# Performance work log

Hardware: AMD Instinct MI355X
Metric: run time of the kernel (lower is better)

The kernel has to match this reference:

```python
import jax, jax.numpy as jnp
import numpy as np

LAYER_NUM = 2
NUM_CLS = 128
HIDDEN = 256
NUM_NODES = 1024


def setup_inputs() -> dict:
    key = jax.random.key(0)
    ks = jax.random.split(key, 12)
    s = 0.05
    return {
        "x": jax.random.normal(ks[0], (NUM_NODES, HIDDEN), jnp.float32),
        "knowledge": jax.random.uniform(ks[1], (NUM_CLS, NUM_CLS), jnp.float32) / NUM_CLS,
        "w3w": jax.random.normal(ks[2], (HIDDEN, 2 * HIDDEN), jnp.float32) * s,
        "b3w": jax.random.normal(ks[3], (HIDDEN,), jnp.float32) * s,
        "u3": jax.random.normal(ks[4], (HIDDEN, HIDDEN), jnp.float32) * s,
        "bu3": jax.random.normal(ks[5], (HIDDEN,), jnp.float32) * s,
        "w4w": jax.random.normal(ks[6], (HIDDEN, 2 * HIDDEN), jnp.float32) * s,
        "b4w": jax.random.normal(ks[7], (HIDDEN,), jnp.float32) * s,
        "w5w": jax.random.normal(ks[8], (HIDDEN, 2 * HIDDEN), jnp.float32) * s,
        "b5w": jax.random.normal(ks[9], (HIDDEN,), jnp.float32) * s,
        "u5": jax.random.normal(ks[10], (HIDDEN, HIDDEN), jnp.float32) * s,
        "bu5": jax.random.normal(ks[11], (HIDDEN,), jnp.float32) * s,
    }


def reference(x, knowledge, w3w, b3w, u3, bu3, w4w, b4w, w5w, b5w, u5, bu5):
    N, H = x.shape
    C = knowledge.shape[0]
    # hidden[n, c, :] = x[n, :]  (repeat per class)
    hidden = jnp.broadcast_to(x[:, None, :], (N, C, H))
    for _ in range(LAYER_NUM):
        hs = hidden.sum(0)                      # [C, H]
        diff = hs[None, :, :] - hidden          # [N, C, H]
        # knowledge.T @ diff_n  and  knowledge @ diff_n, vectorized over nodes
        left = jnp.einsum('kc,nkh->nch', knowledge, diff)
        right = jnp.einsum('ck,nkh->nch', knowledge, diff)
        av = jnp.concatenate([left, right], axis=-1).reshape(N * C, 2 * H)
        h = hidden.reshape(N * C, H)
        uh3 = h @ u3.T + bu3                    # shared: rv uses fc_eq3_u (source quirk)
        zv = jax.nn.sigmoid(av @ w3w.T + b3w + uh3)
        rv = jax.nn.sigmoid(av @ w4w.T + b4w + uh3)
        hv = jnp.tanh(av @ w5w.T + b5w + (rv * h) @ u5.T + bu5)
        h = (1.0 - zv) * h + zv * hv
        hidden = h.reshape(N, C, H)
    return hidden
```

## Files before the change

kernel.cpp:

```cpp
#include <hip/hip_runtime.h>
#include <cstdint>
#include <cstddef>


#define NODES 1024
#define NCLS  128
#define HID   256

using frag  = __attribute__((ext_vector_type(8))) short;
using frag4 = __attribute__((ext_vector_type(4))) short;
using f32x4 = __attribute__((ext_vector_type(4))) float;

__device__ __forceinline__ float bf2f(unsigned short h){
  unsigned int u = ((unsigned int)h) << 16;
  float f; __builtin_memcpy(&f, &u, 4); return f;
}
__device__ __forceinline__ unsigned short f2bf(float f){
  unsigned int u; __builtin_memcpy(&u, &f, 4);
  u = (u + 0x7fffu + ((u >> 16) & 1u)) >> 16;
  return (unsigned short)u;
}
__device__ __forceinline__ float sigm(float x){ return 1.0f/(1.0f + __expf(-x)); }
__device__ __forceinline__ float tanh_fast(float x){ return 1.0f - 2.0f/(__expf(2.0f*x) + 1.0f); }

#define GLOBAL_AS(p) ((const __attribute__((address_space(1))) void*)(p))
#define LDS_AS(p)    ((__attribute__((address_space(3))) void*)(p))

template<int OUT_BF16>
__global__ __launch_bounds__(256) void gemm_bf16(
    const unsigned short* __restrict__ A0, int ldA0, int K0,
    const unsigned short* __restrict__ A1, int ldA1,
    const unsigned short* __restrict__ BT, int ldB, long bStride,
    void* __restrict__ Cptr, int ldC,
    int Ntiles, int Ktot, unsigned int aMask, int Mtiles)
{
  __shared__ unsigned short As[4096];
  __shared__ unsigned short Bs[4096];
  const int t   = threadIdx.x;
  const int bid = blockIdx.x;
  const int xcd = bid & 7, slot = bid >> 3;
  const int mtPerX = (Mtiles >= 8) ? (Mtiles >> 3) : 1;
  const int mt = xcd * mtPerX + slot / Ntiles;
  const int nt = slot % Ntiles;
  const int lane = t & 63, w = t >> 6;
  const int wm = w >> 1, wn = w & 1;
  const int r = lane & 15, q = lane >> 4;
  const int m0 = mt * 128, n0 = nt * 128;
  const unsigned short* Bbase = BT + (size_t)mt * (size_t)bStride;

  f32x4 acc[4][4] = {};

  for (int kb = 0; kb < Ktot; kb += 32) {
#pragma unroll
    for (int i = 0; i < 2; ++i) {
      int u  = i * 256 + t;
      int mi = u >> 2;
      int kc = (u & 3) * 8;
      int k  = kb + kc;
      const unsigned short* ga;
      if (k < K0) ga = A0 + (size_t)((unsigned int)(m0 + mi) & aMask) * (size_t)ldA0 + k;
      else        ga = A1 + (size_t)(m0 + mi) * (size_t)ldA1 + (k - K0);
      __builtin_amdgcn_global_load_lds(GLOBAL_AS(ga), LDS_AS(&As[u * 8]), 16, 0, 0);
      const unsigned short* gb = Bbase + (size_t)(n0 + mi) * (size_t)ldB + k;
      __builtin_amdgcn_global_load_lds(GLOBAL_AS(gb), LDS_AS(&Bs[u * 8]), 16, 0, 0);
    }
    __syncthreads();

    frag af[4], bf_[4];
#pragma unroll
    for (int x = 0; x < 4; ++x) {
      af[x]  = *(const frag*)&As[(wm * 64 + x * 16 + r) * 32 + q * 8];
      bf_[x] = *(const frag*)&Bs[(wn * 64 + x * 16 + r) * 32 + q * 8];
    }
#pragma unroll
    for (int x = 0; x < 4; ++x)
#pragma unroll
      for (int y = 0; y < 4; ++y)
        acc[x][y] = __builtin_amdgcn_mfma_f32_16x16x32_bf16(af[x], bf_[y], acc[x][y], 0, 0, 0);
    __syncthreads();
  }

#pragma unroll
  for (int x = 0; x < 4; ++x) {
#pragma unroll
    for (int y = 0; y < 4; ++y) {
      int col = n0 + wn * 64 + y * 16 + r;
#pragma unroll
      for (int g = 0; g < 4; ++g) {
        long row = m0 + wm * 64 + x * 16 + q * 4 + g;
        if (OUT_BF16) ((unsigned short*)Cptr)[row * (long)ldC + col] = f2bf(acc[x][y][g]);
        else          ((float*)Cptr)[row * (long)ldC + col] = acc[x][y][g];
      }
    }
  }
}

__global__ __launch_bounds__(256, 4) void gemm_pre(
    const unsigned short* __restrict__ AVH, const unsigned short* __restrict__ H1,
    const unsigned short* __restrict__ WB, unsigned short* __restrict__ PRE)
{
  __shared__ __align__(16) unsigned short SM[16384];
  const int t   = threadIdx.x;
  const int bid = blockIdx.x;
  const int xcd = bid & 7, slot = bid >> 3;
  const int mt = xcd * 128 + slot / 6;
  const int ct = slot % 6;
  const int lane = t & 63, w = t >> 6;
  const int wm = w >> 1, wn = w & 1;
  const int r = lane & 15, q = lane >> 4;
  const int m0 = mt * 128;
  const unsigned short* Wrow = WB + (size_t)(ct * 128) * 768;
  const int nst = (ct < 4) ? 24 : 16;

  f32x4 acc[4][4] = {};

  auto STAGE = [&](int b, int kt) {
    const int kb = kt * 32;
    unsigned short* Asb = SM + b * 4096;
    unsigned short* Bsb = SM + 8192 + b * 4096;
#pragma unroll
    for (int i = 0; i < 2; ++i) {
      int u  = i * 256 + t;
      int mi = u >> 2;
      int gc = (u & 3) ^ (mi & 3);
      const unsigned short* ga;
      if (kb < 512) ga = AVH + (size_t)(m0 + mi) * 512 + kb + gc * 8;
      else          ga = H1  + (size_t)(m0 + mi) * 256 + (kb - 512) + gc * 8;
      __builtin_amdgcn_global_load_lds(GLOBAL_AS(ga), LDS_AS(&Asb[u * 8]), 16, 0, 0);
      __builtin_amdgcn_global_load_lds(GLOBAL_AS(Wrow + (size_t)mi * 768 + kb + gc * 8),
                                       LDS_AS(&Bsb[u * 8]), 16, 0, 0);
    }
  };

  STAGE(0, 0);
  __syncthreads();
  int cur = 0;
  for (int kt = 0; kt < nst; ++kt) {
    if (kt + 1 < nst) STAGE(cur ^ 1, kt + 1);
    const unsigned short* Asb = SM + cur * 4096;
    const unsigned short* Bsb = SM + 8192 + cur * 4096;
    frag af[4], bf_[4];
#pragma unroll
    for (int x = 0; x < 4; ++x) {
      int ra = wm * 64 + x * 16 + r;
      int rb = wn * 64 + x * 16 + r;
      af[x]  = *(const frag*)&Asb[ra * 32 + ((q ^ (ra & 3)) * 8)];
      bf_[x] = *(const frag*)&Bsb[rb * 32 + ((q ^ (rb & 3)) * 8)];
    }
#pragma unroll
    for (int x = 0; x < 4; ++x)
#pragma unroll
      for (int y = 0; y < 4; ++y)
        acc[x][y] = __builtin_amdgcn_mfma_f32_16x16x32_bf16(af[x], bf_[y], acc[x][y], 0, 0, 0);
    __syncthreads();
    cur ^= 1;
  }

  unsigned short* L = SM;
#pragma unroll
  for (int x = 0; x < 4; ++x)
#pragma unroll
    for (int y = 0; y < 4; ++y) {
      int j = wn * 64 + y * 16 + r;
#pragma unroll
      for (int g = 0; g < 4; ++g) {
        int c = wm * 64 + x * 16 + q * 4 + g;
        L[c * 128 + (((j >> 3) ^ (c & 7)) * 8) + (j & 7)] = f2bf(acc[x][y][g]);
      }
    }
  __syncthreads();
#pragma unroll
  for (int it = 0; it < 8; ++it) {
    int unit = it * 256 + t;
    int row = unit >> 4, gr = unit & 15;
    frag v = *(const frag*)&L[row * 128 + ((gr ^ (row & 7)) * 8)];
    *(frag*)&PRE[(size_t)(m0 + row) * 768 + ct * 128 + gr * 8] = v;
  }
}

__global__ __launch_bounds__(256) void gemm_l1(
    const float* __restrict__ XW, const float* __restrict__ SW,
    const float* __restrict__ x,
    const float* __restrict__ b3, const float* __restrict__ b4,
    const float* __restrict__ b5, const float* __restrict__ bu3,
    const float* __restrict__ bu5,
    const float* __restrict__ colsum, const float* __restrict__ rowsum,
    const unsigned short* __restrict__ u5b,
    const unsigned short* __restrict__ KTbN, const unsigned short* __restrict__ KbN,
    unsigned short* __restrict__ H1, unsigned short* __restrict__ AVH)
{
  __shared__ unsigned short SM[17408];
  unsigned short* As = SM;
  unsigned short* Bs = SM + 4096;
  unsigned short* L  = SM;
  __shared__ float tP1[256], tP2[256], tP3[256], tX[256];
  __shared__ float tZ1[256], tZ2[256], tZ3[256];
  __shared__ float tV1[256], tV2[256], tV3[256];
  __shared__ float tCS[128], tRS[128];

  const int t = threadIdx.x, bid = blockIdx.x;
  const int xcd = bid & 7, slot = bid >> 3;
  const int n  = xcd * 128 + (slot >> 1);
  const int nt = slot & 1;
  const int lane = t & 63, w = t >> 6, wm = w >> 1, wn = w & 1;
  const int r = lane & 15, q = lane >> 4;
  const int n0 = nt * 128;
  const float* xw = XW + (size_t)n * 1792;

  {
    int i = t;
    float xwi0 = xw[i], xwi1 = xw[256 + i], xwi2 = xw[512 + i], xwi3 = xw[768 + i];
    float xwi4 = xw[1024 + i], xwi5 = xw[1280 + i], xwu = xw[1536 + i];
    tP1[i] = SW[512 + i] - xwi2;
    tP2[i] = SW[768 + i] - xwi3;
    tP3[i] = xwu + b4[i] + bu3[i];
    tX[i]  = x[(size_t)n * HID + i];
    tZ1[i] = SW[i] - xwi0;
    tZ2[i] = SW[256 + i] - xwi1;
    tZ3[i] = xwu + b3[i] + bu3[i];
    tV1[i] = SW[1024 + i] - xwi4;
    tV2[i] = SW[1280 + i] - xwi5;
    tV3[i] = b5[i] + bu5[i];
    if (t < 128) { tCS[t] = colsum[t]; tRS[t] = rowsum[t]; }
  }
  __syncthreads();

  f32x4 acc[4][4] = {};

  for (int kb = 0; kb < 256; kb += 32) {
#pragma unroll
    for (int i = 0; i < 2; ++i) {
      int u  = i * 256 + t;
      int mi = u >> 2;
      int c  = u & 3;
      int kc = c * 8;
      int k  = kb + kc;
      int gc = c ^ (mi & 3);
      __builtin_amdgcn_global_load_lds(GLOBAL_AS(u5b + (size_t)(n0 + mi) * 256 + kb + gc * 8),
                                       LDS_AS(&Bs[u * 8]), 16, 0, 0);
      float cs = tCS[mi], rs = tRS[mi];
      frag a;
#pragma unroll
      for (int e = 0; e < 8; ++e) {
        int i2 = k + e;
        float pre = cs * tP1[i2] + rs * tP2[i2] + tP3[i2];
        a[e] = (short)f2bf(sigm(pre) * tX[i2]);
      }
      *(frag*)&As[mi * 32 + (c ^ (mi & 3)) * 8] = a;
    }
    __syncthreads();

    frag af[4], bf_[4];
#pragma unroll
    for (int xx = 0; xx < 4; ++xx) {
      int ra = wm * 64 + xx * 16 + r;
      int rb = wn * 64 + xx * 16 + r;
      af[xx]  = *(const frag*)&As[ra * 32 + ((q ^ (ra & 3)) * 8)];
      bf_[xx] = *(const frag*)&Bs[rb * 32 + ((q ^ (rb & 3)) * 8)];
    }
#pragma unroll
    for (int xx = 0; xx < 4; ++xx)
#pragma unroll
      for (int y = 0; y < 4; ++y)
        acc[xx][y] = __builtin_amdgcn_mfma_f32_16x16x32_bf16(af[xx], bf_[y], acc[xx][y], 0, 0, 0);
    __syncthreads();
  }

#pragma unroll
  for (int xx = 0; xx < 4; ++xx) {
#pragma unroll
    for (int y = 0; y < 4; ++y) {
      int j = wn * 64 + y * 16 + r;
      int i = n0 + j;
      frag4 pack;
#pragma unroll
      for (int g = 0; g < 4; ++g) {
        int c = wm * 64 + xx * 16 + q * 4 + g;
        float cs = tCS[c], rs = tRS[c];
        float z  = sigm(cs * tZ1[i] + rs * tZ2[i] + tZ3[i]);
        float p5 = cs * tV1[i] + rs * tV2[i] + tV3[i] + acc[xx][y][g];
        float h1 = (1.0f - z) * tX[i] + z * tanh_fast(p5);
        unsigned short hb = f2bf(h1);
        pack[g] = (short)hb;
        H1[(size_t)(n * 128 + c) * HID + i] = hb;
      }
      *(frag4*)&L[j * 136 + (wm * 64 + xx * 16 + q * 4)] = pack;
    }
  }
  __syncthreads();

#pragma unroll
  for (int s = 0; s < 2; ++s) {
    const unsigned short* Ks = s ? KbN : KTbN;
    f32x4 a2[4][4] = {};
#pragma unroll
    for (int kb = 0; kb < 4; ++kb) {
      frag af[4], bf_[4];
#pragma unroll
      for (int xx = 0; xx < 4; ++xx) {
        int cp = wm * 64 + xx * 16 + r;
        af[xx] = *(const frag*)(Ks + (size_t)cp * 128 + kb * 32 + q * 8);
        int j = wn * 64 + xx * 16 + r;
        bf_[xx] = *(const frag*)&L[j * 136 + kb * 32 + q * 8];
      }
#pragma unroll
      for (int xx = 0; xx < 4; ++xx)
#pragma unroll
        for (int y = 0; y < 4; ++y)
          a2[xx][y] = __builtin_amdgcn_mfma_f32_16x16x32_bf16(af[xx], bf_[y], a2[xx][y], 0, 0, 0);
    }
#pragma unroll
    for (int xx = 0; xx < 4; ++xx)
#pragma unroll
      for (int y = 0; y < 4; ++y) {
        int col = s * 256 + n0 + wn * 64 + y * 16 + r;
#pragma unroll
        for (int g = 0; g < 4; ++g) {
          int cp = wm * 64 + xx * 16 + q * 4 + g;
          AVH[(size_t)(n * 128 + cp) * 512 + col] = f2bf(a2[xx][y][g]);
        }
      }
  }
}

__global__ __launch_bounds__(256) void gemm_l2(
    const unsigned short* __restrict__ PRE, const float* __restrict__ SG,
    const unsigned short* __restrict__ H1, const unsigned short* __restrict__ u5b,
    float* __restrict__ out)
{
  __shared__ unsigned short As[4096], Bs[4096];
  const int t = threadIdx.x, bid = blockIdx.x;
  const int xcd = bid & 7, slot = bid >> 3;
  const int mt = xcd * 128 + (slot >> 1);
  const int nt = slot & 1;
  const int lane = t & 63, w = t >> 6, wm = w >> 1, wn = w & 1;
  const int r = lane & 15, q = lane >> 4;
  const int m0 = mt * 128, n0 = nt * 128;

  f32x4 acc[4][4] = {};

  for (int kb = 0; kb < 256; kb += 32) {
#pragma unroll
    for (int i = 0; i < 2; ++i) {
      int u  = i * 256 + t;
      int mi = u >> 2;
      int c  = u & 3;
      int k  = kb + c * 8;
      int gc = c ^ (mi & 3);
      __builtin_amdgcn_global_load_lds(GLOBAL_AS(u5b + (size_t)(n0 + mi) * 256 + kb + gc * 8),
                                       LDS_AS(&Bs[u * 8]), 16, 0, 0);
      long row = m0 + mi;
      frag p4 = *(const frag*)(PRE + row * 768 + 256 + k);
      frag h1 = *(const frag*)(H1 + row * 256 + k);
      const float* sg = SG + (size_t)mi * 768 + 256 + k;
      frag a;
#pragma unroll
      for (int e = 0; e < 8; ++e) {
        float rv = sigm(sg[e] + bf2f((unsigned short)p4[e]));
        a[e] = (short)f2bf(rv * bf2f((unsigned short)h1[e]));
      }
      *(frag*)&As[mi * 32 + (c ^ (mi & 3)) * 8] = a;
    }
    __syncthreads();

    frag af[4], bf_[4];
#pragma unroll
    for (int xx = 0; xx < 4; ++xx) {
      int ra = wm * 64 + xx * 16 + r;
      int rb = wn * 64 + xx * 16 + r;
      af[xx]  = *(const frag*)&As[ra * 32 + ((q ^ (ra & 3)) * 8)];
      bf_[xx] = *(const frag*)&Bs[rb * 32 + ((q ^ (rb & 3)) * 8)];
    }
#pragma unroll
    for (int xx = 0; xx < 4; ++xx)
#pragma unroll
      for (int y = 0; y < 4; ++y)
        acc[xx][y] = __builtin_amdgcn_mfma_f32_16x16x32_bf16(af[xx], bf_[y], acc[xx][y], 0, 0, 0);
    __syncthreads();
  }

#pragma unroll
  for (int xx = 0; xx < 4; ++xx) {
#pragma unroll
    for (int y = 0; y < 4; ++y) {
      int i = n0 + wn * 64 + y * 16 + r;
#pragma unroll
      for (int g = 0; g < 4; ++g) {
        int c = wm * 64 + xx * 16 + q * 4 + g;
        long row = m0 + c;
        float z  = sigm(SG[(size_t)c * 768 + i] + bf2f(PRE[row * 768 + i]));
        float pv = SG[(size_t)c * 768 + 512 + i] + bf2f(PRE[row * 768 + 512 + i])
                 + acc[xx][y][g];
        float h  = bf2f(H1[row * 256 + i]);
        out[row * 256 + i] = (1.0f - z) * h + z * tanh_fast(pv);
      }
    }
  }
}

__global__ __launch_bounds__(256) void prep_cast(
    const float* __restrict__ x, const float* __restrict__ Kn,
    const float* __restrict__ w3, const float* __restrict__ u3,
    const float* __restrict__ w4, const float* __restrict__ w5,
    const float* __restrict__ u5,
    unsigned short* __restrict__ xb, unsigned short* __restrict__ WB,
    unsigned short* __restrict__ WB2, unsigned short* __restrict__ u5b,
    unsigned short* __restrict__ KbN, unsigned short* __restrict__ KTbN)
{
  int idx = blockIdx.x * 256 + threadIdx.x;
  if (idx < 262144) { xb[idx] = f2bf(x[idx]); return; }
  idx -= 262144;
  if (idx < 589824) {
    int col = idx / 768, j = idx % 768;
    int g = col >> 8, i = col & 255;
    float v;
    if (j < 512) { const float* wg = (g == 0) ? w3 : (g == 1) ? w4 : w5; v = wg[(size_t)i * 512 + j]; }
    else v = (g < 2) ? u3[(size_t)i * 256 + (j - 512)] : 0.0f;
    WB[(size_t)col * 768 + j] = f2bf(v);
    return;
  }
  idx -= 589824;
  if (idx < 458752) {
    int col = idx / 256, h = idx % 256;
    int b = col >> 8, i = col & 255;
    float v = (b < 6) ? ((b < 2 ? w3 : (b < 4 ? w4 : w5))[(size_t)i * 512 + (b & 1) * 256 + h])
                      : u3[(size_t)i * 256 + h];
    WB2[(size_t)col * 256 + h] = f2bf(v);
    return;
  }
  idx -= 458752;
  if (idx < 65536) { u5b[idx] = f2bf(u5[idx]); return; }
  idx -= 65536;
  if (idx < 16384) { int c = idx >> 7, k = idx & 127; KbN[idx]  = f2bf(-Kn[c * 128 + k]); return; }
  idx -= 16384;
  { int c = idx >> 7, k = idx & 127; KTbN[idx] = f2bf(-Kn[k * 128 + c]); }
}

__global__ __launch_bounds__(256) void prep_reduce(
    const float* __restrict__ x, const float* __restrict__ Kn,
    float* __restrict__ S, float* __restrict__ colsum, float* __restrict__ rowsum)
{
  int b = blockIdx.x, t = threadIdx.x;
  if (b < 8) {
    float s = 0.f;
    for (int n = 0; n < 128; ++n) s += x[(size_t)(b * 128 + n) * HID + t];
    atomicAdd(&S[t], s);
  } else if (b == 8) {
    if (t < NCLS) { float s = 0.f; for (int k = 0; k < NCLS; ++k) s += Kn[k * NCLS + t]; colsum[t] = s; }
  } else {
    if (t < NCLS) { float s = 0.f; for (int k = 0; k < NCLS; ++k) s += Kn[t * NCLS + k]; rowsum[t] = s; }
  }
}

__global__ __launch_bounds__(256) void prep_sw(
    const float* __restrict__ S, const float* __restrict__ w3,
    const float* __restrict__ w4, const float* __restrict__ w5, float* __restrict__ SW)
{
  int col = blockIdx.x * 256 + threadIdx.x;
  int b = col >> 8, i = col & 255;
  const float* w = (b < 2) ? w3 : (b < 4) ? w4 : w5;
  const float* row = w + (size_t)i * 512 + (b & 1) * 256;
  float s = 0.f;
  for (int h = 0; h < HID; ++h) s += S[h] * row[h];
  SW[col] = s;
}

__global__ __launch_bounds__(256) void reduce_hs(
    const unsigned short* __restrict__ H1, float* __restrict__ hs)
{
  int bid = blockIdx.x;
  int c = bid >> 5, nch = bid & 31;
  int i = threadIdx.x;
  const unsigned short* p = H1 + (size_t)nch * 32 * NCLS * HID + (size_t)c * HID + i;
  float s = 0.f;
  for (int n = 0; n < 32; ++n) s += bf2f(p[(size_t)n * NCLS * HID]);
  atomicAdd(&hs[c * HID + i], s);
}

__global__ __launch_bounds__(256) void p2a(
    const float* __restrict__ hs, const float* __restrict__ w3,
    const float* __restrict__ w4, const float* __restrict__ w5, float* __restrict__ hsW)
{
  __shared__ float hrow[HID];
  int k = blockIdx.x & 127, b = blockIdx.x >> 7;
  int t = threadIdx.x;
  hrow[t] = hs[k * HID + t];
  __syncthreads();
  const float* w = (b < 2) ? w3 : (b < 4) ? w4 : w5;
  const float* row = w + (size_t)t * 512 + (b & 1) * 256;
  float s = 0.f;
  for (int h = 0; h < HID; ++h) s += hrow[h] * row[h];
  hsW[(size_t)k * 1536 + b * 256 + t] = s;
}

__global__ __launch_bounds__(256) void p2b(
    const float* __restrict__ hsW, const float* __restrict__ Kn,
    const float* __restrict__ b3, const float* __restrict__ b4, const float* __restrict__ b5,
    const float* __restrict__ bu3, const float* __restrict__ bu5, float* __restrict__ SG)
{
  __shared__ float kc[NCLS], kr[NCLS];
  int c = blockIdx.x, t = threadIdx.x;
  if (t < NCLS) { kc[t] = Kn[t * NCLS + c]; kr[t] = Kn[c * NCLS + t]; }
  __syncthreads();
  for (int g = 0; g < 3; ++g) {
    int i = t;
    const float* L = hsW + (size_t)(2 * g) * 256 + i;
    const float* R = hsW + (size_t)(2 * g + 1) * 256 + i;
    float s = 0.f;
    for (int k = 0; k < NCLS; ++k) s += kc[k] * L[(size_t)k * 1536] + kr[k] * R[(size_t)k * 1536];
    const float* bg = (g == 0) ? b3 : (g == 1) ? b4 : b5;
    s += bg[i] + ((g < 2) ? bu3[i] : bu5[i]);
    SG[(size_t)c * 768 + g * 256 + i] = s;
  }
}

extern "C" void kernel_launch(void* const* d_in, const int* in_sizes, int n_in,
                              void* d_out, int out_size, void* d_ws, size_t ws_size,
                              hipStream_t stream) {
  (void)in_sizes; (void)n_in; (void)out_size; (void)ws_size;
  const float* x   = (const float*)d_in[0];
  const float* Kn  = (const float*)d_in[1];
  const float* w3  = (const float*)d_in[2];
  const float* b3  = (const float*)d_in[3];
  const float* u3  = (const float*)d_in[4];
  const float* bu3 = (const float*)d_in[5];
  const float* w4  = (const float*)d_in[6];
  const float* b4  = (const float*)d_in[7];
  const float* w5  = (const float*)d_in[8];
  const float* b5  = (const float*)d_in[9];
  const float* u5  = (const float*)d_in[10];
  const float* bu5 = (const float*)d_in[11];
  float* out = (float*)d_out;

  char* w = (char*)d_ws;
  unsigned short* AVH = (unsigned short*)(w);
  unsigned short* PRE = (unsigned short*)(w + 134217728);
  unsigned short* H1  = (unsigned short*)(w + 335544320);
  float*          XW  = (float*)(w + 402653184);
  char* misc = w + 409993216;
  float* S      = (float*)(misc);
  float* hs     = (float*)(misc + 1024);
  float* SW     = (float*)(misc + 132096);
  float* colsum = (float*)(misc + 138240);
  float* rowsum = (float*)(misc + 138752);
  float* hsW    = (float*)(misc + 139264);
  float* SG     = (float*)(misc + 925696);
  unsigned short* WB   = (unsigned short*)(misc + 1318912);
  unsigned short* WB2  = (unsigned short*)(misc + 2498560);
  unsigned short* u5b  = (unsigned short*)(misc + 3416064);
  unsigned short* KbN  = (unsigned short*)(misc + 3547136);
  unsigned short* KTbN = (unsigned short*)(misc + 3579904);
  unsigned short* xb   = (unsigned short*)(misc + 3612672);

  hipMemsetAsync(misc, 0, 132096, stream);

  prep_cast<<<5504, 256, 0, stream>>>(x, Kn, w3, u3, w4, w5, u5, xb, WB, WB2, u5b, KbN, KTbN);
  prep_reduce<<<10, 256, 0, stream>>>(x, Kn, S, colsum, rowsum);
  prep_sw<<<6, 256, 0, stream>>>(S, w3, w4, w5, SW);

  gemm_bf16<0><<<8 * 14, 256, 0, stream>>>(xb, 256, 256, xb, 256, WB2, 256, 0L,
                                           (void*)XW, 1792, 14, 256, 0xFFFFFFFFu, 8);
  gemm_l1<<<2048, 256, 0, stream>>>(XW, SW, x, b3, b4, b5, bu3, bu5,
                                    colsum, rowsum, u5b, KTbN, KbN, H1, AVH);

  reduce_hs<<<4096, 256, 0, stream>>>(H1, hs);
  p2a<<<768, 256, 0, stream>>>(hs, w3, w4, w5, hsW);
  p2b<<<128, 256, 0, stream>>>(hsW, Kn, b3, b4, b5, bu3, bu5, SG);

  gemm_pre<<<6144, 256, 0, stream>>>(AVH, H1, WB, PRE);

  gemm_l2<<<2048, 256, 0, stream>>>(PRE, SG, H1, u5b, out);
}
```

Baseline: 709.9 us.

## Double-buffer B tiles with vmcnt-based waits and retune LDS swizzle

Adds double-buffered async global-to-LDS staging of the u5 weight tiles in gemm_l1 and gemm_l2, so the next tile's load overlaps the current tile's MFMA work. The heavy __syncthreads calls become raw s_barrier plus explicit s_waitcnt vmcnt/lgkmcnt counts, letting one prefetch stay in flight. gemm_l2 also batches its activation loads before the compute loop. The LDS XOR swizzle changes to use (row>>1)&3 and c&12 to cut bank conflicts. The hand-written waitcnt counts are fragile: a wrong count would allow a read of LDS before the data has landed.

```diff
diff --git a/kernel.cpp b/kernel.cpp
--- a/kernel.cpp
+++ b/kernel.cpp
@@ -122,7 +122,7 @@
     for (int i = 0; i < 2; ++i) {
       int u  = i * 256 + t;
       int mi = u >> 2;
-      int gc = (u & 3) ^ (mi & 3);
+      int gc = (u & 3) ^ ((mi >> 1) & 3);
       const unsigned short* ga;
       if (kb < 512) ga = AVH + (size_t)(m0 + mi) * 512 + kb + gc * 8;
       else          ga = H1  + (size_t)(m0 + mi) * 256 + (kb - 512) + gc * 8;
@@ -133,10 +133,16 @@
   };
 
   STAGE(0, 0);
-  __syncthreads();
   int cur = 0;
   for (int kt = 0; kt < nst; ++kt) {
-    if (kt + 1 < nst) STAGE(cur ^ 1, kt + 1);
+    if (kt + 1 < nst) {
+      STAGE(cur ^ 1, kt + 1);
+      asm volatile("s_waitcnt vmcnt(4)" ::: "memory");
+    } else {
+      asm volatile("s_waitcnt vmcnt(0)" ::: "memory");
+    }
+    __builtin_amdgcn_s_barrier();
+    asm volatile("" ::: "memory");
     const unsigned short* Asb = SM + cur * 4096;
     const unsigned short* Bsb = SM + 8192 + cur * 4096;
     frag af[4], bf_[4];
@@ -144,15 +150,16 @@
     for (int x = 0; x < 4; ++x) {
       int ra = wm * 64 + x * 16 + r;
       int rb = wn * 64 + x * 16 + r;
-      af[x]  = *(const frag*)&Asb[ra * 32 + ((q ^ (ra & 3)) * 8)];
-      bf_[x] = *(const frag*)&Bsb[rb * 32 + ((q ^ (rb & 3)) * 8)];
+      af[x]  = *(const frag*)&Asb[ra * 32 + ((q ^ ((ra >> 1) & 3)) * 8)];
+      bf_[x] = *(const frag*)&Bsb[rb * 32 + ((q ^ ((rb >> 1) & 3)) * 8)];
     }
 #pragma unroll
     for (int x = 0; x < 4; ++x)
 #pragma unroll
       for (int y = 0; y < 4; ++y)
         acc[x][y] = __builtin_amdgcn_mfma_f32_16x16x32_bf16(af[x], bf_[y], acc[x][y], 0, 0, 0);
-    __syncthreads();
+    asm volatile("" ::: "memory");
+    __builtin_amdgcn_s_barrier();
     cur ^= 1;
   }
 
@@ -165,7 +172,7 @@
 #pragma unroll
       for (int g = 0; g < 4; ++g) {
         int c = wm * 64 + x * 16 + q * 4 + g;
-        L[c * 128 + (((j >> 3) ^ (c & 7)) * 8) + (j & 7)] = f2bf(acc[x][y][g]);
+        L[c * 128 + (((j >> 3) ^ (c & 12)) * 8) + (j & 7)] = f2bf(acc[x][y][g]);
       }
     }
   __syncthreads();
@@ -173,7 +180,7 @@
   for (int it = 0; it < 8; ++it) {
     int unit = it * 256 + t;
     int row = unit >> 4, gr = unit & 15;
-    frag v = *(const frag*)&L[row * 128 + ((gr ^ (row & 7)) * 8)];
+    frag v = *(const frag*)&L[row * 128 + ((gr ^ (row & 12)) * 8)];
     *(frag*)&PRE[(size_t)(m0 + row) * 768 + ct * 128 + gr * 8] = v;
   }
 }
@@ -191,7 +198,6 @@
 {
   __shared__ unsigned short SM[17408];
   unsigned short* As = SM;
-  unsigned short* Bs = SM + 4096;
   unsigned short* L  = SM;
   __shared__ float tP1[256], tP2[256], tP3[256], tX[256];
   __shared__ float tZ1[256], tZ2[256], tZ3[256];
@@ -206,6 +212,18 @@
   const int r = lane & 15, q = lane >> 4;
   const int n0 = nt * 128;
   const float* xw = XW + (size_t)n * 1792;
+
+  auto STAGE_B = [&](int b, int kb) {
+    unsigned short* Bsb = SM + 4096 + b * 4096;
+#pragma unroll
+    for (int i = 0; i < 2; ++i) {
+      int u  = i * 256 + t;
+      int mi = u >> 2;
+      int gc = (u & 3) ^ ((mi >> 1) & 3);
+      __builtin_amdgcn_global_load_lds(GLOBAL_AS(u5b + (size_t)(n0 + mi) * 256 + kb + gc * 8),
+                                       LDS_AS(&Bsb[u * 8]), 16, 0, 0);
+    }
+  };
 
   {
     int i = t;
@@ -223,21 +241,22 @@
     tV3[i] = b5[i] + bu5[i];
     if (t < 128) { tCS[t] = colsum[t]; tRS[t] = rowsum[t]; }
   }
-  __syncthreads();
+  STAGE_B(0, 0);
+  asm volatile("s_waitcnt lgkmcnt(0)" ::: "memory");
+  __builtin_amdgcn_s_barrier();
+  asm volatile("" ::: "memory");
 
   f32x4 acc[4][4] = {};
 
+  int cur = 0;
   for (int kb = 0; kb < 256; kb += 32) {
+    if (kb < 224) STAGE_B(cur ^ 1, kb + 32);
 #pragma unroll
     for (int i = 0; i < 2; ++i) {
       int u  = i * 256 + t;
       int mi = u >> 2;
       int c  = u & 3;
-      int kc = c * 8;
-      int k  = kb + kc;
-      int gc = c ^ (mi & 3);
-      __builtin_amdgcn_global_load_lds(GLOBAL_AS(u5b + (size_t)(n0 + mi) * 256 + kb + gc * 8),
-                                       LDS_AS(&Bs[u * 8]), 16, 0, 0);
+      int k  = kb + c * 8;
       float cs = tCS[mi], rs = tRS[mi];
       frag a;
 #pragma unroll
@@ -246,24 +265,30 @@
         float pre = cs * tP1[i2] + rs * tP2[i2] + tP3[i2];
         a[e] = (short)f2bf(sigm(pre) * tX[i2]);
       }
-      *(frag*)&As[mi * 32 + (c ^ (mi & 3)) * 8] = a;
-    }
-    __syncthreads();
-
+      *(frag*)&As[mi * 32 + ((c ^ ((mi >> 1) & 3)) * 8)] = a;
+    }
+    if (kb < 224) asm volatile("s_waitcnt vmcnt(2) lgkmcnt(0)" ::: "memory");
+    else          asm volatile("s_waitcnt vmcnt(0) lgkmcnt(0)" ::: "memory");
+    __builtin_amdgcn_s_barrier();
+    asm volatile("" ::: "memory");
+
+    const unsigned short* Bsb = SM + 4096 + cur * 4096;
     frag af[4], bf_[4];
 #pragma unroll
     for (int xx = 0; xx < 4; ++xx) {
       int ra = wm * 64 + xx * 16 + r;
       int rb = wn * 64 + xx * 16 + r;
-      af[xx]  = *(const frag*)&As[ra * 32 + ((q ^ (ra & 3)) * 8)];
-      bf_[xx] = *(const frag*)&Bs[rb * 32 + ((q ^ (rb & 3)) * 8)];
+      af[xx]  = *(const frag*)&As[ra * 32 + ((q ^ ((ra >> 1) & 3)) * 8)];
+      bf_[xx] = *(const frag*)&Bsb[rb * 32 + ((q ^ ((rb >> 1) & 3)) * 8)];
     }
 #pragma unroll
     for (int xx = 0; xx < 4; ++xx)
 #pragma unroll
       for (int y = 0; y < 4; ++y)
         acc[xx][y] = __builtin_amdgcn_mfma_f32_16x16x32_bf16(af[xx], bf_[y], acc[xx][y], 0, 0, 0);
-    __syncthreads();
+    asm volatile("" ::: "memory");
+    __builtin_amdgcn_s_barrier();
+    cur ^= 1;
   }
 
 #pragma unroll
@@ -328,7 +353,7 @@
     const unsigned short* __restrict__ H1, const unsigned short* __restrict__ u5b,
     float* __restrict__ out)
 {
-  __shared__ unsigned short As[4096], Bs[4096];
+  __shared__ unsigned short As[4096], Bs[8192];
   const int t = threadIdx.x, bid = blockIdx.x;
   const int xcd = bid & 7, slot = bid >> 3;
   const int mt = xcd * 128 + (slot >> 1);
@@ -337,46 +362,74 @@
   const int r = lane & 15, q = lane >> 4;
   const int m0 = mt * 128, n0 = nt * 128;
 
+  auto STAGE_B = [&](int b, int kb) {
+    unsigned short* Bsb = Bs + b * 4096;
+#pragma unroll
+    for (int i = 0; i < 2; ++i) {
+      int u  = i * 256 + t;
+      int mi = u >> 2;
+      int gc = (u & 3) ^ ((mi >> 1) & 3);
+      __builtin_amdgcn_global_load_lds(GLOBAL_AS(u5b + (size_t)(n0 + mi) * 256 + kb + gc * 8),
+                                       LDS_AS(&Bsb[u * 8]), 16, 0, 0);
+    }
+  };
+
   f32x4 acc[4][4] = {};
 
+  STAGE_B(0, 0);
+  int cur = 0;
   for (int kb = 0; kb < 256; kb += 32) {
+    frag p4a[2], h1a[2];
+    f32x4 sga[2][2];
 #pragma unroll
     for (int i = 0; i < 2; ++i) {
       int u  = i * 256 + t;
       int mi = u >> 2;
       int c  = u & 3;
       int k  = kb + c * 8;
-      int gc = c ^ (mi & 3);
-      __builtin_amdgcn_global_load_lds(GLOBAL_AS(u5b + (size_t)(n0 + mi) * 256 + kb + gc * 8),
-                                       LDS_AS(&Bs[u * 8]), 16, 0, 0);
       long row = m0 + mi;
-      frag p4 = *(const frag*)(PRE + row * 768 + 256 + k);
-      frag h1 = *(const frag*)(H1 + row * 256 + k);
-      const float* sg = SG + (size_t)mi * 768 + 256 + k;
+      p4a[i] = *(const frag*)(PRE + row * 768 + 256 + k);
+      h1a[i] = *(const frag*)(H1 + row * 256 + k);
+      sga[i][0] = *(const f32x4*)(SG + (size_t)mi * 768 + 256 + k);
+      sga[i][1] = *(const f32x4*)(SG + (size_t)mi * 768 + 256 + k + 4);
+    }
+    if (kb < 224) STAGE_B(cur ^ 1, kb + 32);
+#pragma unroll
+    for (int i = 0; i < 2; ++i) {
+      int u  = i * 256 + t;
+      int mi = u >> 2;
+      int c  = u & 3;
       frag a;
 #pragma unroll
       for (int e = 0; e < 8; ++e) {
-        float rv = sigm(sg[e] + bf2f((unsigned short)p4[e]));
-        a[e] = (short)f2bf(rv * bf2f((unsigned short)h1[e]));
-      }
-      *(frag*)&As[mi * 32 + (c ^ (mi & 3)) * 8] = a;
-    }
-    __syncthreads();
-
+        float sgv = (e < 4) ? sga[i][0][e] : sga[i][1][e - 4];
+        float rv = sigm(sgv + bf2f((unsigned short)p4a[i][e]));
+        a[e] = (short)f2bf(rv * bf2f((unsigned short)h1a[i][e]));
+      }
+      *(frag*)&As[mi * 32 + ((c ^ ((mi >> 1) & 3)) * 8)] = a;
+    }
+    if (kb < 224) asm volatile("s_waitcnt vmcnt(2) lgkmcnt(0)" ::: "memory");
+    else          asm volatile("s_waitcnt vmcnt(0) lgkmcnt(0)" ::: "memory");
+    __builtin_amdgcn_s_barrier();
+    asm volatile("" ::: "memory");
+
+    const unsigned short* Bsb = Bs + cur * 4096;
     frag af[4], bf_[4];
 #pragma unroll
     for (int xx = 0; xx < 4; ++xx) {
       int ra = wm * 64 + xx * 16 + r;
       int rb = wn * 64 + xx * 16 + r;
-      af[xx]  = *(const frag*)&As[ra * 32 + ((q ^ (ra & 3)) * 8)];
-      bf_[xx] = *(const frag*)&Bs[rb * 32 + ((q ^ (rb & 3)) * 8)];
+      af[xx]  = *(const frag*)&As[ra * 32 + ((q ^ ((ra >> 1) & 3)) * 8)];
+      bf_[xx] = *(const frag*)&Bsb[rb * 32 + ((q ^ ((rb >> 1) & 3)) * 8)];
     }
 #pragma unroll
     for (int xx = 0; xx < 4; ++xx)
 #pragma unroll
       for (int y = 0; y < 4; ++y)
         acc[xx][y] = __builtin_amdgcn_mfma_f32_16x16x32_bf16(af[xx], bf_[y], acc[xx][y], 0, 0, 0);
-    __syncthreads();
+    asm volatile("" ::: "memory");
+    __builtin_amdgcn_s_barrier();
+    cur ^= 1;
   }
 
 #pragma unroll
```

New measurement: 760.9 us. +7.2%, slower.
